# Optimization experiments

Hardware: AMD Instinct MI355X
Metric: run time of the kernel (lower is better)

## Reference

```python
import jax, jax.numpy as jnp
import numpy as np


def setup_inputs() -> dict:
    key = jax.random.key(0)
    k_in, k_w = jax.random.split(key)
    input = jax.random.normal(k_in, (16, 64, 64, 512), dtype=jnp.float32)
    weight = jax.random.normal(k_w, (512, 512), dtype=jnp.float32)
    return {"input": input, "weight": weight}


def reference(input, weight):
    # Faithful to the torch source, including its quirky (weight*weight).sum(0)
    # (sum over the vocab axis -> (embed_dim,) vector, broadcast over vocab
    # columns; valid here because vocab_size == embed_dim).
    batch_dims, embed_dim = input.shape[:-1], input.shape[-1]
    x = input.reshape(-1, embed_dim)                     # (N, D)
    dists = -2.0 * jnp.einsum("nd,vd->nv", x, weight) + jnp.sum(weight * weight, axis=0)[None, :]
    idxes = jnp.argmin(dists, axis=1)                    # (N,)
    values = weight[idxes].reshape(*batch_dims, embed_dim)
    return values
```

## Files before the change

kernel.cpp:

```cpp
#include <hip/hip_runtime.h>


#define DIM   512
#define VOCAB 512
#define EPS_GAP 0.03f

typedef float f32x4 __attribute__((ext_vector_type(4)));
typedef short bf16x8 __attribute__((ext_vector_type(8)));
typedef unsigned long long u64;

__device__ inline unsigned short f2bf(float f){
    unsigned u = __float_as_uint(f);
    return (unsigned short)((u + 0x7fffu + ((u >> 16) & 1u)) >> 16);
}
__device__ inline float bf2f(unsigned short h){
    return __uint_as_float(((unsigned)h) << 16);
}
__device__ inline u64 packkey(float s, int v){
    unsigned u = __float_as_uint(s);
    u = (u & 0x80000000u) ? ~u : (u | 0x80000000u);
    return (((u64)u) << 32) | (unsigned)(~v);
}
__device__ inline float keyscore(u64 k){
    unsigned e = (unsigned)(k >> 32);
    return __uint_as_float((e & 0x80000000u) ? (e & 0x7fffffffu) : ~e);
}
__device__ inline int keyv(u64 k){ return (int)(~(unsigned)(k & 0xffffffffu)); }
__device__ inline u64 umax64(u64 a, u64 b){ return a > b ? a : b; }
__device__ inline u64 umin64(u64 a, u64 b){ return a < b ? a : b; }

__global__ void colsumsq_kernel(const float* __restrict__ w, float* __restrict__ c){
    const int v = blockIdx.x;
    const int lane = threadIdx.x;
    double s = 0.0;
    for (int i = lane; i < DIM; i += 64){
        const float wv = w[i * VOCAB + v];
        s += (double)wv * (double)wv;
    }
    #pragma unroll
    for (int m = 1; m <= 32; m <<= 1) s += __shfl_xor(s, m, 64);
    if (lane == 0) c[v] = (float)s;
}

__global__ void prep_w(const float* __restrict__ w,
                       unsigned short* __restrict__ whc,
                       unsigned short* __restrict__ wlc,
                       unsigned* __restrict__ cnt){
    const int i = blockIdx.x * 256 + threadIdx.x;
    const float f = w[i];
    const unsigned short h = f2bf(f);
    const unsigned short l = f2bf(f - bf2f(h));
    const int v = i >> 9, k = i & 511;
    const int d = (k >> 5) * 16384 + ((k >> 3) & 3) * 4096 + v * 8 + (k & 7);
    whc[d] = h; wlc[d] = l;
    if (i == 0) *cnt = 0u;
}

__launch_bounds__(256, 2)
__global__ void k1_scores(const float* __restrict__ x,
                          const unsigned short* __restrict__ whc,
                          const unsigned short* __restrict__ wlc,
                          const float* __restrict__ cg,
                          const float* __restrict__ w,
                          float* __restrict__ out,
                          int* __restrict__ list,
                          unsigned* __restrict__ cnt){
    __shared__ __align__(16) unsigned short Ah[16384];
    __shared__ __align__(16) unsigned short Al[16384];
    __shared__ u64 mergeK[64][4][2];
    __shared__ int idx_s[64];

    const int t = threadIdx.x;
    const int lane = t & 63, wv = t >> 6, quad = lane >> 4, lm = lane & 15;
    const int cb = wv << 7;
    const long rbase = (long)blockIdx.x * 64;
    const float* xblk = x + rbase * DIM;

    f32x4 acc[4][8];
    #pragma unroll
    for (int ct = 0; ct < 8; ++ct){
        const float bias = -0.5f * cg[cb + ct * 16 + lm];
        f32x4 z; z[0] = bias; z[1] = bias; z[2] = bias; z[3] = bias;
        #pragma unroll
        for (int rt = 0; rt < 4; ++rt) acc[rt][ct] = z;
    }

    for (int half = 0; half < 2; ++half){
        __syncthreads();
        #pragma unroll 8
        for (int jj = 0; jj < 16; ++jj){
            const int j   = jj * 256 + t;
            const int row = (j >> 3) & 63;
            const int k4  = (j & 7) | ((j >> 9) << 3);
            const int kk  = k4 << 2;
            const float4 a4 = *(const float4*)(xblk + (long)row * DIM + half * 256 + kk);
            ushort4 h4, l4;
            h4.x = f2bf(a4.x); l4.x = f2bf(a4.x - bf2f(h4.x));
            h4.y = f2bf(a4.y); l4.y = f2bf(a4.y - bf2f(h4.y));
            h4.z = f2bf(a4.z); l4.z = f2bf(a4.z - bf2f(h4.z));
            h4.w = f2bf(a4.w); l4.w = f2bf(a4.w - bf2f(h4.w));
            const int d = (((kk >> 5) * 4 + ((kk >> 3) & 3)) * 64 + row) * 8 + (kk & 7);
            *(ushort4*)&Ah[d] = h4;
            *(ushort4*)&Al[d] = l4;
        }
        __syncthreads();

        for (int ch2 = 0; ch2 < 8; ++ch2){
            const int ch = half * 8 + ch2;
            bf16x8 ah[4], al[4];
            #pragma unroll
            for (int rt = 0; rt < 4; ++rt){
                const int d = ((ch2 * 4 + quad) * 64 + rt * 16 + lm) * 8;
                ah[rt] = *(const bf16x8*)&Ah[d];
                al[rt] = *(const bf16x8*)&Al[d];
            }
            const unsigned short* bbh = whc + ch * 16384 + quad * 4096;
            const unsigned short* bbl = wlc + ch * 16384 + quad * 4096;
            #pragma unroll
            for (int ct = 0; ct < 8; ++ct){
                const int co = (cb + ct * 16 + lm) * 8;
                const bf16x8 bh = *(const bf16x8*)(bbh + co);
                const bf16x8 bl = *(const bf16x8*)(bbl + co);
                #pragma unroll
                for (int rt = 0; rt < 4; ++rt){
                    f32x4 a = acc[rt][ct];
                    a = __builtin_amdgcn_mfma_f32_16x16x32_bf16(ah[rt], bh, a, 0, 0, 0);
                    a = __builtin_amdgcn_mfma_f32_16x16x32_bf16(al[rt], bh, a, 0, 0, 0);
                    a = __builtin_amdgcn_mfma_f32_16x16x32_bf16(ah[rt], bl, a, 0, 0, 0);
                    acc[rt][ct] = a;
                }
            }
        }
    }

    #pragma unroll
    for (int rt = 0; rt < 4; ++rt){
        #pragma unroll
        for (int reg = 0; reg < 4; ++reg){
            u64 b1 = 0, b2 = 0;
            #pragma unroll
            for (int ct = 0; ct < 8; ++ct){
                const u64 key = packkey(acc[rt][ct][reg], cb + ct * 16 + lm);
                if (key > b1){ b2 = b1; b1 = key; }
                else if (key > b2){ b2 = key; }
            }
            #pragma unroll
            for (int m = 1; m <= 8; m <<= 1){
                const u64 o1 = __shfl_xor(b1, m, 64);
                const u64 o2 = __shfl_xor(b2, m, 64);
                const u64 n1 = umax64(b1, o1);
                b2 = umax64(umin64(b1, o1), umax64(b2, o2));
                b1 = n1;
            }
            if (lm == 0){
                const int row = rt * 16 + quad * 4 + reg;
                mergeK[row][wv][0] = b1;
                mergeK[row][wv][1] = b2;
            }
        }
    }
    __syncthreads();
    if (t < 64){
        u64 p1 = mergeK[t][0][0], p2 = mergeK[t][0][1];
        #pragma unroll
        for (int i = 1; i < 4; ++i){
            const u64 q1 = mergeK[t][i][0], q2 = mergeK[t][i][1];
            const u64 n1 = umax64(p1, q1);
            p2 = umax64(umin64(p1, q1), umax64(p2, q2));
            p1 = n1;
        }
        idx_s[t] = keyv(p1);
        if (keyscore(p1) - keyscore(p2) < EPS_GAP){
            const unsigned p = atomicAdd(cnt, 1u);
            list[p] = (int)(rbase + t);
        }
    }
    __syncthreads();

    for (int rr = 0; rr < 64; rr += 2){
        const int row  = rr + (t >> 7);
        const int col  = (t & 127) << 2;
        const int vidx = idx_s[row];
        const float4 val = *(const float4*)(w + (long)vidx * DIM + col);
        *(float4*)(out + (rbase + row) * DIM + col) = val;
    }
}

__global__ void refine_rows(const float* __restrict__ x, const float* __restrict__ w,
                            const float* __restrict__ cg, const int* __restrict__ list,
                            const unsigned* __restrict__ cnt, float* __restrict__ out){
    __shared__ float xs[DIM];
    __shared__ u64 wk[4];
    __shared__ int bestv_s;
    const int t = threadIdx.x;
    const int n = (int)*cnt;
    for (int i = blockIdx.x; i < n; i += gridDim.x){
        const int row = list[i];
        __syncthreads();
        if (t < 128) *(float4*)&xs[t * 4] = *(const float4*)(x + (long)row * DIM + t * 4);
        __syncthreads();
        u64 best = 0;
        #pragma unroll
        for (int vv = 0; vv < 2; ++vv){
            const int v = t + vv * 256;
            const float* wr = w + (long)v * DIM;
            float s = 0.f;
            for (int k = 0; k < DIM; k += 4){
                const float4 w4 = *(const float4*)(wr + k);
                s = fmaf(w4.x, xs[k + 0], s);
                s = fmaf(w4.y, xs[k + 1], s);
                s = fmaf(w4.z, xs[k + 2], s);
                s = fmaf(w4.w, xs[k + 3], s);
            }
            s -= 0.5f * cg[v];
            best = umax64(best, packkey(s, v));
        }
        #pragma unroll
        for (int m = 1; m <= 32; m <<= 1) best = umax64(best, __shfl_xor(best, m, 64));
        if ((t & 63) == 0) wk[t >> 6] = best;
        __syncthreads();
        if (t == 0){
            const u64 b = umax64(umax64(wk[0], wk[1]), umax64(wk[2], wk[3]));
            bestv_s = keyv(b);
        }
        __syncthreads();
        const int bv = bestv_s;
        if (t < 128)
            *(float4*)(out + (long)row * DIM + t * 4) =
                *(const float4*)(w + (long)bv * DIM + t * 4);
    }
}

__launch_bounds__(256)
__global__ void fallback_full(const float* __restrict__ x, const float* __restrict__ w,
                              float* __restrict__ out){
    __shared__ __align__(16) float As[16][68];
    __shared__ __align__(16) float Bs[16][VOCAB];
    __shared__ int   idx_sf[64];
    __shared__ float c_s[VOCAB];

    const int t  = threadIdx.x;
    const int tx = t & 31;
    const int ty = t >> 5;
    const long rbase = (long)blockIdx.x * 64;
    const float* xblk = x + rbase * DIM;

    for (int vv = t; vv < VOCAB; vv += 256){
        double s = 0.0;
        for (int i = 0; i < DIM; ++i){
            const float wvv = w[i * VOCAB + vv];
            s += (double)wvv * (double)wvv;
        }
        c_s[vv] = (float)s;
    }

    float acc[8][16];
    #pragma unroll
    for (int r = 0; r < 8; ++r)
        #pragma unroll
        for (int j = 0; j < 16; ++j) acc[r][j] = 0.0f;

    for (int k0 = 0; k0 < DIM; k0 += 16){
        __syncthreads();
        {
            const int r  = t >> 2;
            const int kq = (t & 3) << 2;
            const float4 a4 = *(const float4*)(xblk + (long)r * DIM + k0 + kq);
            As[kq + 0][r] = a4.x; As[kq + 1][r] = a4.y;
            As[kq + 2][r] = a4.z; As[kq + 3][r] = a4.w;
        }
        #pragma unroll
        for (int vb = 0; vb < 8; ++vb){
            const int v  = (t >> 2) + (vb << 6);
            const int kq = (t & 3) << 2;
            const float4 b4 = *(const float4*)(w + (long)v * DIM + k0 + kq);
            Bs[kq + 0][v] = b4.x; Bs[kq + 1][v] = b4.y;
            Bs[kq + 2][v] = b4.z; Bs[kq + 3][v] = b4.w;
        }
        __syncthreads();

        #pragma unroll
        for (int k = 0; k < 16; ++k){
            float a[8];
            const float4 a03 = *(const float4*)&As[k][ty * 8];
            const float4 a47 = *(const float4*)&As[k][ty * 8 + 4];
            a[0] = a03.x; a[1] = a03.y; a[2] = a03.z; a[3] = a03.w;
            a[4] = a47.x; a[5] = a47.y; a[6] = a47.z; a[7] = a47.w;
            float b[16];
            #pragma unroll
            for (int j = 0; j < 16; ++j) b[j] = Bs[k][tx + (j << 5)];
            #pragma unroll
            for (int r = 0; r < 8; ++r)
                #pragma unroll
                for (int j = 0; j < 16; ++j)
                    acc[r][j] = fmaf(a[r], b[j], acc[r][j]);
        }
    }

    #pragma unroll
    for (int r = 0; r < 8; ++r){
        float best = acc[r][0] - 0.5f * c_s[tx];
        int   bv   = tx;
        #pragma unroll
        for (int j = 1; j < 16; ++j){
            const float s = acc[r][j] - 0.5f * c_s[tx + (j << 5)];
            if (s > best){ best = s; bv = tx + (j << 5); }
        }
        unsigned u = __float_as_uint(best);
        u = (u & 0x80000000u) ? ~u : (u | 0x80000000u);
        u64 key = ((u64)u << 32) | (unsigned)(~(unsigned)bv);
        #pragma unroll
        for (int m = 1; m <= 16; m <<= 1){
            const u64 o = __shfl_xor(key, m, 64);
            if (o > key) key = o;
        }
        if (tx == 0) idx_sf[ty * 8 + r] = (int)(~(unsigned)(key & 0xFFFFFFFFull));
    }
    __syncthreads();

    for (int rr = 0; rr < 64; rr += 2){
        const int row  = rr + (t >> 7);
        const int col  = (t & 127) << 2;
        const int vidx = idx_sf[row];
        const float4 val = *(const float4*)(w + (long)vidx * DIM + col);
        *(float4*)(out + (rbase + row) * DIM + col) = val;
    }
}

extern "C" void kernel_launch(void* const* d_in, const int* in_sizes, int n_in,
                              void* d_out, int out_size, void* d_ws, size_t ws_size,
                              hipStream_t stream){
    const float* x = (const float*)d_in[0];
    const float* w = (const float*)d_in[1];
    float* out = (float*)d_out;
    const int rows = in_sizes[0] / DIM;

    const size_t whc_off  = 0;
    const size_t wlc_off  = whc_off + (size_t)DIM * VOCAB * 2;
    const size_t c_off    = wlc_off + (size_t)DIM * VOCAB * 2;
    const size_t list_off = c_off   + (size_t)VOCAB * 4;
    const size_t cnt_off  = list_off + (size_t)rows * 4;
    const size_t need     = cnt_off + 16;

    if (ws_size >= need){
        unsigned short* whc = (unsigned short*)((char*)d_ws + whc_off);
        unsigned short* wlc = (unsigned short*)((char*)d_ws + wlc_off);
        float*    c    = (float*)((char*)d_ws + c_off);
        int*      list = (int*)((char*)d_ws + list_off);
        unsigned* cnt  = (unsigned*)((char*)d_ws + cnt_off);

        prep_w<<<(DIM * VOCAB) / 256, 256, 0, stream>>>(w, whc, wlc, cnt);
        colsumsq_kernel<<<VOCAB, 64, 0, stream>>>(w, c);
        k1_scores<<<rows / 64, 256, 0, stream>>>(x, whc, wlc, c, w, out, list, cnt);
        refine_rows<<<512, 256, 0, stream>>>(x, w, c, list, cnt, out);
    } else {
        fallback_full<<<rows / 64, 256, 0, stream>>>(x, w, out);
    }
}
```

Baseline: 355.8 us.

## Switch coarse scoring to single fp16 MFMA pass with wider refine margin and batched refine

The coarse scoring kernel drops the three-pass bf16 hi/lo split and runs one fp16 MFMA pass per tile. It loads activations straight from global memory into registers with a one-chunk prefetch instead of staging them through shared memory, and uses 32-row blocks with higher occupancy. To make up for the lower precision, the ambiguity gap that sends rows to exact fp32 rescoring is widened, so more rows go through refinement. The refine kernel now handles 8 rows per block so each weight row it loads is reused across several rows. The risk is a much larger refine workload, and fp16 could overflow or lose accuracy if the inputs had a different scale.

Result: no change. 354.8 us (-0.3%).

```diff
diff --git a/kernel.cpp b/kernel.cpp
--- a/kernel.cpp
+++ b/kernel.cpp
@@ -3,19 +3,13 @@
 
 #define DIM   512
 #define VOCAB 512
-#define EPS_GAP 0.03f
+#define EPS_GAP 0.18f
+#define RBATCH 8
 
 typedef float f32x4 __attribute__((ext_vector_type(4)));
-typedef short bf16x8 __attribute__((ext_vector_type(8)));
+typedef _Float16 f16x8 __attribute__((ext_vector_type(8)));
 typedef unsigned long long u64;
 
-__device__ inline unsigned short f2bf(float f){
-    unsigned u = __float_as_uint(f);
-    return (unsigned short)((u + 0x7fffu + ((u >> 16) & 1u)) >> 16);
-}
-__device__ inline float bf2f(unsigned short h){
-    return __uint_as_float(((unsigned)h) << 16);
-}
 __device__ inline u64 packkey(float s, int v){
     unsigned u = __float_as_uint(s);
     u = (u & 0x80000000u) ? ~u : (u | 0x80000000u);
@@ -43,98 +37,73 @@
 }
 
 __global__ void prep_w(const float* __restrict__ w,
-                       unsigned short* __restrict__ whc,
-                       unsigned short* __restrict__ wlc,
+                       _Float16* __restrict__ whc,
                        unsigned* __restrict__ cnt){
     const int i = blockIdx.x * 256 + threadIdx.x;
-    const float f = w[i];
-    const unsigned short h = f2bf(f);
-    const unsigned short l = f2bf(f - bf2f(h));
     const int v = i >> 9, k = i & 511;
     const int d = (k >> 5) * 16384 + ((k >> 3) & 3) * 4096 + v * 8 + (k & 7);
-    whc[d] = h; wlc[d] = l;
+    whc[d] = (_Float16)w[i];
     if (i == 0) *cnt = 0u;
 }
 
-__launch_bounds__(256, 2)
+__launch_bounds__(256, 3)
 __global__ void k1_scores(const float* __restrict__ x,
-                          const unsigned short* __restrict__ whc,
-                          const unsigned short* __restrict__ wlc,
+                          const _Float16* __restrict__ whc,
                           const float* __restrict__ cg,
                           const float* __restrict__ w,
                           float* __restrict__ out,
                           int* __restrict__ list,
                           unsigned* __restrict__ cnt){
-    __shared__ __align__(16) unsigned short Ah[16384];
-    __shared__ __align__(16) unsigned short Al[16384];
-    __shared__ u64 mergeK[64][4][2];
-    __shared__ int idx_s[64];
+    __shared__ u64 mergeK[32][4][2];
+    __shared__ int idx_s[32];
 
     const int t = threadIdx.x;
     const int lane = t & 63, wv = t >> 6, quad = lane >> 4, lm = lane & 15;
     const int cb = wv << 7;
-    const long rbase = (long)blockIdx.x * 64;
+    const long rbase = (long)blockIdx.x * 32;
     const float* xblk = x + rbase * DIM;
 
-    f32x4 acc[4][8];
+    f32x4 acc[2][8];
     #pragma unroll
     for (int ct = 0; ct < 8; ++ct){
         const float bias = -0.5f * cg[cb + ct * 16 + lm];
         f32x4 z; z[0] = bias; z[1] = bias; z[2] = bias; z[3] = bias;
-        #pragma unroll
-        for (int rt = 0; rt < 4; ++rt) acc[rt][ct] = z;
-    }
-
-    for (int half = 0; half < 2; ++half){
-        __syncthreads();
-        #pragma unroll 8
-        for (int jj = 0; jj < 16; ++jj){
-            const int j   = jj * 256 + t;
-            const int row = (j >> 3) & 63;
-            const int k4  = (j & 7) | ((j >> 9) << 3);
-            const int kk  = k4 << 2;
-            const float4 a4 = *(const float4*)(xblk + (long)row * DIM + half * 256 + kk);
-            ushort4 h4, l4;
-            h4.x = f2bf(a4.x); l4.x = f2bf(a4.x - bf2f(h4.x));
-            h4.y = f2bf(a4.y); l4.y = f2bf(a4.y - bf2f(h4.y));
-            h4.z = f2bf(a4.z); l4.z = f2bf(a4.z - bf2f(h4.z));
-            h4.w = f2bf(a4.w); l4.w = f2bf(a4.w - bf2f(h4.w));
-            const int d = (((kk >> 5) * 4 + ((kk >> 3) & 3)) * 64 + row) * 8 + (kk & 7);
-            *(ushort4*)&Ah[d] = h4;
-            *(ushort4*)&Al[d] = l4;
-        }
-        __syncthreads();
-
-        for (int ch2 = 0; ch2 < 8; ++ch2){
-            const int ch = half * 8 + ch2;
-            bf16x8 ah[4], al[4];
-            #pragma unroll
-            for (int rt = 0; rt < 4; ++rt){
-                const int d = ((ch2 * 4 + quad) * 64 + rt * 16 + lm) * 8;
-                ah[rt] = *(const bf16x8*)&Ah[d];
-                al[rt] = *(const bf16x8*)&Al[d];
-            }
-            const unsigned short* bbh = whc + ch * 16384 + quad * 4096;
-            const unsigned short* bbl = wlc + ch * 16384 + quad * 4096;
-            #pragma unroll
-            for (int ct = 0; ct < 8; ++ct){
-                const int co = (cb + ct * 16 + lm) * 8;
-                const bf16x8 bh = *(const bf16x8*)(bbh + co);
-                const bf16x8 bl = *(const bf16x8*)(bbl + co);
-                #pragma unroll
-                for (int rt = 0; rt < 4; ++rt){
-                    f32x4 a = acc[rt][ct];
-                    a = __builtin_amdgcn_mfma_f32_16x16x32_bf16(ah[rt], bh, a, 0, 0, 0);
-                    a = __builtin_amdgcn_mfma_f32_16x16x32_bf16(al[rt], bh, a, 0, 0, 0);
-                    a = __builtin_amdgcn_mfma_f32_16x16x32_bf16(ah[rt], bl, a, 0, 0, 0);
-                    acc[rt][ct] = a;
-                }
-            }
-        }
-    }
-
-    #pragma unroll
-    for (int rt = 0; rt < 4; ++rt){
+        acc[0][ct] = z; acc[1][ct] = z;
+    }
+
+    const float* ap0 = xblk + (long)(lm)      * DIM + quad * 8;
+    const float* ap1 = xblk + (long)(16 + lm) * DIM + quad * 8;
+
+    float4 ar0a = *(const float4*)(ap0);
+    float4 ar0b = *(const float4*)(ap0 + 4);
+    float4 ar1a = *(const float4*)(ap1);
+    float4 ar1b = *(const float4*)(ap1 + 4);
+
+    #pragma unroll 1
+    for (int ch = 0; ch < 16; ++ch){
+        f16x8 ah0, ah1;
+        ah0[0]=(_Float16)ar0a.x; ah0[1]=(_Float16)ar0a.y; ah0[2]=(_Float16)ar0a.z; ah0[3]=(_Float16)ar0a.w;
+        ah0[4]=(_Float16)ar0b.x; ah0[5]=(_Float16)ar0b.y; ah0[6]=(_Float16)ar0b.z; ah0[7]=(_Float16)ar0b.w;
+        ah1[0]=(_Float16)ar1a.x; ah1[1]=(_Float16)ar1a.y; ah1[2]=(_Float16)ar1a.z; ah1[3]=(_Float16)ar1a.w;
+        ah1[4]=(_Float16)ar1b.x; ah1[5]=(_Float16)ar1b.y; ah1[6]=(_Float16)ar1b.z; ah1[7]=(_Float16)ar1b.w;
+
+        const int chn = (ch < 15) ? ch + 1 : 15;
+        ar0a = *(const float4*)(ap0 + chn * 32);
+        ar0b = *(const float4*)(ap0 + chn * 32 + 4);
+        ar1a = *(const float4*)(ap1 + chn * 32);
+        ar1b = *(const float4*)(ap1 + chn * 32 + 4);
+
+        const _Float16* bb = whc + ch * 16384 + quad * 4096 + (cb + lm) * 8;
+        #pragma unroll
+        for (int ct = 0; ct < 8; ++ct){
+            const f16x8 bh = *(const f16x8*)(bb + ct * 128);
+            acc[0][ct] = __builtin_amdgcn_mfma_f32_16x16x32_f16(ah0, bh, acc[0][ct], 0, 0, 0);
+            acc[1][ct] = __builtin_amdgcn_mfma_f32_16x16x32_f16(ah1, bh, acc[1][ct], 0, 0, 0);
+        }
+    }
+
+    #pragma unroll
+    for (int rt = 0; rt < 2; ++rt){
         #pragma unroll
         for (int reg = 0; reg < 4; ++reg){
             u64 b1 = 0, b2 = 0;
@@ -160,7 +129,7 @@
         }
     }
     __syncthreads();
-    if (t < 64){
+    if (t < 32){
         u64 p1 = mergeK[t][0][0], p2 = mergeK[t][0][1];
         #pragma unroll
         for (int i = 1; i < 4; ++i){
@@ -177,7 +146,7 @@
     }
     __syncthreads();
 
-    for (int rr = 0; rr < 64; rr += 2){
+    for (int rr = 0; rr < 32; rr += 2){
         const int row  = rr + (t >> 7);
         const int col  = (t & 127) << 2;
         const int vidx = idx_s[row];
@@ -189,45 +158,63 @@
 __global__ void refine_rows(const float* __restrict__ x, const float* __restrict__ w,
                             const float* __restrict__ cg, const int* __restrict__ list,
                             const unsigned* __restrict__ cnt, float* __restrict__ out){
-    __shared__ float xs[DIM];
-    __shared__ u64 wk[4];
-    __shared__ int bestv_s;
+    __shared__ __align__(16) float xs[RBATCH][DIM];
+    __shared__ u64 wk[RBATCH][4];
+    __shared__ int bestv_s[RBATCH];
     const int t = threadIdx.x;
+    const int lane = t & 63, wvq = t >> 6;
     const int n = (int)*cnt;
-    for (int i = blockIdx.x; i < n; i += gridDim.x){
-        const int row = list[i];
-        __syncthreads();
-        if (t < 128) *(float4*)&xs[t * 4] = *(const float4*)(x + (long)row * DIM + t * 4);
-        __syncthreads();
-        u64 best = 0;
+    for (int base = blockIdx.x * RBATCH; base < n; base += gridDim.x * RBATCH){
+        const int m = (n - base < RBATCH) ? (n - base) : RBATCH;
+        __syncthreads();
+        for (int s = t; s < m * 128; s += 256){
+            const int r = s >> 7, c = (s & 127) << 2;
+            *(float4*)&xs[r][c] = *(const float4*)(x + (long)list[base + r] * DIM + c);
+        }
+        __syncthreads();
+        u64 best[RBATCH];
+        #pragma unroll
+        for (int r = 0; r < RBATCH; ++r) best[r] = 0;
         #pragma unroll
         for (int vv = 0; vv < 2; ++vv){
             const int v = t + vv * 256;
             const float* wr = w + (long)v * DIM;
-            float s = 0.f;
+            float s[RBATCH];
+            #pragma unroll
+            for (int r = 0; r < RBATCH; ++r) s[r] = -0.5f * cg[v];
             for (int k = 0; k < DIM; k += 4){
                 const float4 w4 = *(const float4*)(wr + k);
-                s = fmaf(w4.x, xs[k + 0], s);
-                s = fmaf(w4.y, xs[k + 1], s);
-                s = fmaf(w4.z, xs[k + 2], s);
-                s = fmaf(w4.w, xs[k + 3], s);
+                #pragma unroll
+                for (int r = 0; r < RBATCH; ++r){
+                    const float4 x4 = *(const float4*)&xs[r][k];
+                    s[r] = fmaf(w4.x, x4.x, s[r]);
+                    s[r] = fmaf(w4.y, x4.y, s[r]);
+                    s[r] = fmaf(w4.z, x4.z, s[r]);
+                    s[r] = fmaf(w4.w, x4.w, s[r]);
+                }
             }
-            s -= 0.5f * cg[v];
-            best = umax64(best, packkey(s, v));
-        }
-        #pragma unroll
-        for (int m = 1; m <= 32; m <<= 1) best = umax64(best, __shfl_xor(best, m, 64));
-        if ((t & 63) == 0) wk[t >> 6] = best;
-        __syncthreads();
-        if (t == 0){
-            const u64 b = umax64(umax64(wk[0], wk[1]), umax64(wk[2], wk[3]));
-            bestv_s = keyv(b);
-        }
-        __syncthreads();
-        const int bv = bestv_s;
-        if (t < 128)
-            *(float4*)(out + (long)row * DIM + t * 4) =
-                *(const float4*)(w + (long)bv * DIM + t * 4);
+            #pragma unroll
+            for (int r = 0; r < RBATCH; ++r)
+                best[r] = umax64(best[r], packkey(s[r], v));
+        }
+        #pragma unroll
+        for (int r = 0; r < RBATCH; ++r){
+            u64 b = best[r];
+            #pragma unroll
+            for (int mm = 1; mm <= 32; mm <<= 1) b = umax64(b, __shfl_xor(b, mm, 64));
+            if (lane == 0) wk[r][wvq] = b;
+        }
+        __syncthreads();
+        if (t < RBATCH){
+            const u64 b = umax64(umax64(wk[t][0], wk[t][1]), umax64(wk[t][2], wk[t][3]));
+            bestv_s[t] = keyv(b);
+        }
+        __syncthreads();
+        for (int s = t; s < m * 128; s += 256){
+            const int r = s >> 7, c = (s & 127) << 2;
+            *(float4*)(out + (long)list[base + r] * DIM + c) =
+                *(const float4*)(w + (long)bestv_s[r] * DIM + c);
+        }
     }
 }
 
@@ -336,22 +323,20 @@
     const int rows = in_sizes[0] / DIM;
 
     const size_t whc_off  = 0;
-    const size_t wlc_off  = whc_off + (size_t)DIM * VOCAB * 2;
-    const size_t c_off    = wlc_off + (size_t)DIM * VOCAB * 2;
+    const size_t c_off    = whc_off + (size_t)DIM * VOCAB * 2;
     const size_t list_off = c_off   + (size_t)VOCAB * 4;
     const size_t cnt_off  = list_off + (size_t)rows * 4;
     const size_t need     = cnt_off + 16;
 
     if (ws_size >= need){
-        unsigned short* whc = (unsigned short*)((char*)d_ws + whc_off);
-        unsigned short* wlc = (unsigned short*)((char*)d_ws + wlc_off);
+        _Float16* whc  = (_Float16*)((char*)d_ws + whc_off);
         float*    c    = (float*)((char*)d_ws + c_off);
         int*      list = (int*)((char*)d_ws + list_off);
         unsigned* cnt  = (unsigned*)((char*)d_ws + cnt_off);
 
-        prep_w<<<(DIM * VOCAB) / 256, 256, 0, stream>>>(w, whc, wlc, cnt);
+        prep_w<<<(DIM * VOCAB) / 256, 256, 0, stream>>>(w, whc, cnt);
         colsumsq_kernel<<<VOCAB, 64, 0, stream>>>(w, c);
-        k1_scores<<<rows / 64, 256, 0, stream>>>(x, whc, wlc, c, w, out, list, cnt);
+        k1_scores<<<rows / 32, 256, 0, stream>>>(x, whc, c, w, out, list, cnt);
         refine_rows<<<512, 256, 0, stream>>>(x, w, c, list, cnt, out);
     } else {
         fallback_full<<<rows / 64, 256, 0, stream>>>(x, w, out);
```
